# Kernel optimization log

Measured on AMD Instinct MI355X. Metric: run time of the kernel, lower is better.

Reference implementation:

```python
import jax, jax.numpy as jnp
import numpy as np

B, T, J, C = 8, 243, 17, 512
H = 8
HD = C // H  # 64
SCALE = HD ** -0.5


def setup_inputs() -> dict:
    key = jax.random.key(0)
    ks = jax.random.split(key, 6)
    x = jax.random.normal(ks[0], (B, T, J, C), dtype=jnp.float32)
    # external attention map, broadcast-compatible with [B,H,J,T,T]; make it row-normalized like a softmax
    am = jax.random.uniform(ks[1], (B, H, J, T, T), dtype=jnp.float32)
    att_map = am / jnp.sum(am, axis=-1, keepdims=True)
    weight = jax.random.uniform(ks[2], (1,), dtype=jnp.float32)
    w_qkv = jax.random.normal(ks[3], (3 * C, C), dtype=jnp.float32) * 0.02
    w_proj = jax.random.normal(ks[4], (C, C), dtype=jnp.float32) * 0.02
    b_proj = jax.random.normal(ks[5], (C,), dtype=jnp.float32) * 0.02
    return {"x": x, "att_map": att_map, "weight": weight,
            "w_qkv": w_qkv, "w_proj": w_proj, "b_proj": b_proj}


def reference(x, att_map, weight, w_qkv, w_proj, b_proj):
    b, t, j, c = x.shape
    h, hd = H, c // H
    # qkv projection (no bias): [B,T,J,3C] -> [3,B,H,T,J,hd]
    qkv = jnp.einsum('btjc,dc->btjd', x, w_qkv).reshape(b, t, j, 3, h, hd)
    qkv = jnp.transpose(qkv, (3, 0, 4, 1, 2, 5))
    q, k, v = qkv[0], qkv[1], qkv[2]
    # transpose T <-> J: attention runs over the temporal axis per joint
    qt = jnp.swapaxes(q, 2, 3)  # [B,H,J,T,hd]
    kt = jnp.swapaxes(k, 2, 3)
    vt = jnp.swapaxes(v, 2, 3)
    attn = jnp.einsum('bhjtc,bhjsc->bhjts', qt, kt) * SCALE  # [B,H,J,T,T]
    attn = jax.nn.softmax(attn, axis=-1)
    # blend with external attention map (dropout p=0.0 -> identity)
    attn = weight * attn + (1.0 - weight) * att_map
    out = jnp.einsum('bhjts,bhjsc->bhjtc', attn, vt)  # [B,H,J,T,hd]
    out = jnp.transpose(out, (0, 3, 2, 1, 4)).reshape(b, t, j, c)  # [B,T,J,C]
    out = out @ w_proj.T + b_proj
    return out
```

## Files before the change

kernel.cpp:

```cpp
#include <hip/hip_runtime.h>
#include <hip/hip_bf16.h>

#define B_ 8
#define T_ 243
#define J_ 17
#define C_ 512
#define H_ 8
#define HD_ 64
#define M_ (B_*T_*J_)
#define SCALE_ 0.125f
#define QKV_ELEMS (B_*H_*J_*T_*HD_)

typedef __attribute__((ext_vector_type(4))) float f32x4;
typedef __attribute__((ext_vector_type(8))) short bf16x8;

__device__ __forceinline__ ushort f2bf(float f) {
  union { float f; unsigned u; } v; v.f = f;
  unsigned r = v.u + 0x7FFFu + ((v.u >> 16) & 1u);
  return (ushort)(r >> 16);
}
__device__ __forceinline__ float bf2f(ushort u) {
  union { unsigned u; float f; } v; v.u = (unsigned)u << 16; return v.f;
}

__global__ __launch_bounds__(256) void cvt_kernel(const float* __restrict__ in,
                                                  ushort* __restrict__ out, int n8) {
  int i = blockIdx.x * 256 + threadIdx.x;
  if (i >= n8) return;
  const float4* p = (const float4*)in + (size_t)i * 2;
  float4 v0 = p[0], v1 = p[1];
  bf16x8 o;
  o[0] = (short)f2bf(v0.x); o[1] = (short)f2bf(v0.y);
  o[2] = (short)f2bf(v0.z); o[3] = (short)f2bf(v0.w);
  o[4] = (short)f2bf(v1.x); o[5] = (short)f2bf(v1.y);
  o[6] = (short)f2bf(v1.z); o[7] = (short)f2bf(v1.w);
  *(bf16x8*)(out + (size_t)i * 8) = o;
}

template<int EPI>
__global__ __launch_bounds__(256) void gemm_bt(
    const ushort* __restrict__ A, const ushort* __restrict__ Bm,
    ushort* __restrict__ qkvout, float* __restrict__ fout,
    const float* __restrict__ bias)
{
  __shared__ ushort As[128 * 64];
  __shared__ ushort Bs[128 * 64];
  const int tid = threadIdx.x;
  const int lane = tid & 63;
  const int lo = lane & 15, hi = lane >> 4;
  const int wave = tid >> 6;
  const int wr = wave >> 1, wc = wave & 1;
  const int mt = blockIdx.x, nt = blockIdx.y;

  f32x4 acc[4][4] = {};

  for (int ks = 0; ks < 8; ++ks) {
    const int k0 = ks * 64;
    bf16x8 ra[4], rb[4];
    #pragma unroll
    for (int i = 0; i < 4; ++i) {
      int c = tid + i * 256;
      int row = c >> 3, col8 = c & 7;
      int arow = mt * 128 + row; if (arow > M_ - 1) arow = M_ - 1;
      ra[i] = *(const bf16x8*)(A + (size_t)arow * 512 + k0 + col8 * 8);
      int brow = nt * 128 + row;
      rb[i] = *(const bf16x8*)(Bm + (size_t)brow * 512 + k0 + col8 * 8);
    }
    __syncthreads();
    #pragma unroll
    for (int i = 0; i < 4; ++i) {
      int c = tid + i * 256;
      int row = c >> 3, col8 = c & 7;
      int sc = col8 ^ (row & 7);
      *(bf16x8*)(As + row * 64 + sc * 8) = ra[i];
      *(bf16x8*)(Bs + row * 64 + sc * 8) = rb[i];
    }
    __syncthreads();
    #pragma unroll
    for (int kk = 0; kk < 2; ++kk) {
      bf16x8 af[4], bf[4];
      #pragma unroll
      for (int mf = 0; mf < 4; ++mf) {
        int row = wr * 64 + mf * 16 + lo;
        int sc = (kk * 4 + hi) ^ (row & 7);
        af[mf] = *(const bf16x8*)(As + row * 64 + sc * 8);
      }
      #pragma unroll
      for (int nf = 0; nf < 4; ++nf) {
        int row = wc * 64 + nf * 16 + lo;
        int sc = (kk * 4 + hi) ^ (row & 7);
        bf[nf] = *(const bf16x8*)(Bs + row * 64 + sc * 8);
      }
      #pragma unroll
      for (int mf = 0; mf < 4; ++mf)
        #pragma unroll
        for (int nf = 0; nf < 4; ++nf)
          acc[mf][nf] = __builtin_amdgcn_mfma_f32_16x16x32_bf16(af[mf], bf[nf], acc[mf][nf], 0, 0, 0);
    }
  }

  if (EPI == 0) {
    const int which = nt >> 2;
    const int h = (nt * 2 + wc) & 7;
    const float scale = (which == 0) ? SCALE_ : 1.0f;
    ushort* basep = qkvout + (size_t)which * QKV_ELEMS;
    #pragma unroll
    for (int mf = 0; mf < 4; ++mf) {
      #pragma unroll
      for (int i = 0; i < 4; ++i) {
        int r = mt * 128 + wr * 64 + mf * 16 + hi * 4 + i;
        if (r >= M_) continue;
        int b = r / (T_ * J_);
        int rem = r - b * (T_ * J_);
        int t = rem / J_;
        int j = rem - t * J_;
        size_t rowoff = (((size_t)(b * H_ + h) * J_ + j) * T_ + t) * HD_;
        #pragma unroll
        for (int nf = 0; nf < 4; ++nf) {
          int hd = nf * 16 + lo;
          basep[rowoff + hd] = f2bf(acc[mf][nf][i] * scale);
        }
      }
    }
  } else {
    #pragma unroll
    for (int mf = 0; mf < 4; ++mf) {
      #pragma unroll
      for (int i = 0; i < 4; ++i) {
        int r = mt * 128 + wr * 64 + mf * 16 + hi * 4 + i;
        if (r >= M_) continue;
        #pragma unroll
        for (int nf = 0; nf < 4; ++nf) {
          int n = nt * 128 + wc * 64 + nf * 16 + lo;
          fout[(size_t)r * C_ + n] = acc[mf][nf][i] + bias[n];
        }
      }
    }
  }
}

__global__ __launch_bounds__(256, 3) void flash_kernel(
    const ushort* __restrict__ q, const ushort* __restrict__ k,
    const ushort* __restrict__ v, const float* __restrict__ wptr,
    ushort* __restrict__ O2)
{
  __shared__ ushort Vt[64 * 256];
  __shared__ ushort Ps[64 * 128];
  __shared__ float red0[2][64];
  __shared__ float red1[2][64];

  const int tid = threadIdx.x;
  const int lane = tid & 63;
  const int lo = lane & 15, hi = lane >> 4;
  const int wave = tid >> 6;
  const int wr = wave >> 1, wc = wave & 1;
  const int bid = blockIdx.x;
  const int workid = (bid & 7) * 544 + (bid >> 3);
  const int bhj = workid >> 2, rt = workid & 3;
  const float w = wptr[0];
  const size_t kvbase = (size_t)bhj * (T_ * HD_);
  const int r0 = rt * 64;

  #pragma unroll
  for (int it = 0; it < 8; ++it) {
    int c = tid + it * 256;
    int s = c >> 3, hd0 = (c & 7) * 8;
    bf16x8 val = {};
    if (s < T_) val = *(const bf16x8*)(v + kvbase + (size_t)s * HD_ + hd0);
    #pragma unroll
    for (int e = 0; e < 8; ++e) {
      int row = hd0 + e;
      int chunk = (s >> 3) ^ (row & 7);
      Vt[row * 256 + chunk * 8 + (s & 7)] = (ushort)val[e];
    }
  }
  __syncthreads();

  bf16x8 aq[2][2];
  #pragma unroll
  for (int mf = 0; mf < 2; ++mf) {
    int t = r0 + wr * 32 + mf * 16 + lo; if (t > T_ - 1) t = T_ - 1;
    #pragma unroll
    for (int kk = 0; kk < 2; ++kk)
      aq[mf][kk] = *(const bf16x8*)(q + kvbase + (size_t)t * HD_ + kk * 32 + hi * 8);
  }

  f32x4 acc[2][8] = {};
  #pragma unroll
  for (int nf = 0; nf < 8; ++nf) {
    int s = wc * 128 + nf * 16 + lo; if (s > T_ - 1) s = T_ - 1;
    #pragma unroll
    for (int kk = 0; kk < 2; ++kk) {
      bf16x8 bk = *(const bf16x8*)(k + kvbase + (size_t)s * HD_ + kk * 32 + hi * 8);
      #pragma unroll
      for (int mf = 0; mf < 2; ++mf)
        acc[mf][nf] = __builtin_amdgcn_mfma_f32_16x16x32_bf16(aq[mf][kk], bk, acc[mf][nf], 0, 0, 0);
    }
  }

  float rmax[2][4];
  #pragma unroll
  for (int mf = 0; mf < 2; ++mf)
    #pragma unroll
    for (int i = 0; i < 4; ++i) {
      float m = -1e30f;
      #pragma unroll
      for (int nf = 0; nf < 8; ++nf) {
        int s = wc * 128 + nf * 16 + lo;
        if (s < T_) m = fmaxf(m, acc[mf][nf][i]);
      }
      rmax[mf][i] = m;
    }
  #pragma unroll
  for (int d = 1; d < 16; d <<= 1)
    #pragma unroll
    for (int mf = 0; mf < 2; ++mf)
      #pragma unroll
      for (int i = 0; i < 4; ++i)
        rmax[mf][i] = fmaxf(rmax[mf][i], __shfl_xor(rmax[mf][i], d, 64));
  if (lo == 0) {
    #pragma unroll
    for (int mf = 0; mf < 2; ++mf)
      #pragma unroll
      for (int i = 0; i < 4; ++i)
        red0[wc][wr * 32 + mf * 16 + hi * 4 + i] = rmax[mf][i];
  }
  __syncthreads();

  float rsum[2][4];
  #pragma unroll
  for (int mf = 0; mf < 2; ++mf)
    #pragma unroll
    for (int i = 0; i < 4; ++i) {
      float Mx = fmaxf(rmax[mf][i], red0[wc ^ 1][wr * 32 + mf * 16 + hi * 4 + i]);
      float ssum = 0.f;
      #pragma unroll
      for (int nf = 0; nf < 8; ++nf) {
        int s = wc * 128 + nf * 16 + lo;
        float e = 0.f;
        if (s < T_) e = __expf(acc[mf][nf][i] - Mx);
        acc[mf][nf][i] = e;
        ssum += e;
      }
      rsum[mf][i] = ssum;
    }
  #pragma unroll
  for (int d = 1; d < 16; d <<= 1)
    #pragma unroll
    for (int mf = 0; mf < 2; ++mf)
      #pragma unroll
      for (int i = 0; i < 4; ++i)
        rsum[mf][i] += __shfl_xor(rsum[mf][i], d, 64);
  if (lo == 0) {
    #pragma unroll
    for (int mf = 0; mf < 2; ++mf)
      #pragma unroll
      for (int i = 0; i < 4; ++i)
        red1[wc][wr * 32 + mf * 16 + hi * 4 + i] = rsum[mf][i];
  }
  __syncthreads();

  float pinv[2][4];
  #pragma unroll
  for (int mf = 0; mf < 2; ++mf)
    #pragma unroll
    for (int i = 0; i < 4; ++i) {
      float L = rsum[mf][i] + red1[wc ^ 1][wr * 32 + mf * 16 + hi * 4 + i];
      pinv[mf][i] = w / L;
    }

  f32x4 oacc[2][2] = {};
  #pragma unroll
  for (int h2 = 0; h2 < 2; ++h2) {
    __syncthreads();
    if (wc == h2) {
      #pragma unroll
      for (int mf = 0; mf < 2; ++mf)
        #pragma unroll
        for (int i = 0; i < 4; ++i) {
          int row_local = wr * 32 + mf * 16 + hi * 4 + i;
          float pw = pinv[mf][i];
          #pragma unroll
          for (int nf = 0; nf < 8; ++nf) {
            int s = h2 * 128 + nf * 16 + lo;
            float p = (s < T_) ? acc[mf][nf][i] * pw : 0.f;
            int s_local = nf * 16 + lo;
            int chunk = (s_local >> 3) ^ (row_local & 7);
            Ps[row_local * 128 + chunk * 8 + (s_local & 7)] = f2bf(p);
          }
        }
    }
    __syncthreads();
    #pragma unroll
    for (int kk = 0; kk < 4; ++kk) {
      bf16x8 ap[2], bv[2];
      #pragma unroll
      for (int mf = 0; mf < 2; ++mf) {
        int row = wr * 32 + mf * 16 + lo;
        int chunk = (kk * 4 + hi) ^ (row & 7);
        ap[mf] = *(const bf16x8*)(Ps + row * 128 + chunk * 8);
      }
      #pragma unroll
      for (int nf = 0; nf < 2; ++nf) {
        int row = wc * 32 + nf * 16 + lo;
        int chunk = ((h2 * 4 + kk) * 4 + hi) ^ (row & 7);
        bv[nf] = *(const bf16x8*)(Vt + row * 256 + chunk * 8);
      }
      #pragma unroll
      for (int mf = 0; mf < 2; ++mf)
        #pragma unroll
        for (int nf = 0; nf < 2; ++nf)
          oacc[mf][nf] = __builtin_amdgcn_mfma_f32_16x16x32_bf16(ap[mf], bv[nf], oacc[mf][nf], 0, 0, 0);
    }
  }

  #pragma unroll
  for (int mf = 0; mf < 2; ++mf)
    #pragma unroll
    for (int i = 0; i < 4; ++i) {
      int t = r0 + wr * 32 + mf * 16 + hi * 4 + i;
      if (t >= T_) continue;
      size_t rowoff = ((size_t)bhj * T_ + t) * HD_;
      #pragma unroll
      for (int nf = 0; nf < 2; ++nf) {
        int hd = wc * 32 + nf * 16 + lo;
        O2[rowoff + hd] = f2bf(oacc[mf][nf][i]);
      }
    }
}

__global__ __launch_bounds__(256, 4) void amv_kernel(
    const float* __restrict__ am, const ushort* __restrict__ v,
    const ushort* __restrict__ o2, const float* __restrict__ wptr,
    ushort* __restrict__ outO)
{
  __shared__ ushort Vt[64 * 256];

  const int tid = threadIdx.x;
  const int lane = tid & 63;
  const int lo = lane & 15, hi = lane >> 4;
  const int wave = tid >> 6;
  const int wr = wave >> 1, wc = wave & 1;
  const int bid = blockIdx.x;
  const int workid = (bid & 7) * 544 + (bid >> 3);
  const int bhj = workid >> 2, rt = workid & 3;
  const int bh = bhj / J_, j = bhj - bh * J_;
  const int b = bh >> 3, h = bh & 7;
  const float wb = 1.0f - wptr[0];
  const size_t kvbase = (size_t)bhj * (T_ * HD_);
  const int r0 = rt * 64;

  #pragma unroll
  for (int it = 0; it < 8; ++it) {
    int c = tid + it * 256;
    int s = c >> 3, hd0 = (c & 7) * 8;
    bf16x8 val = {};
    if (s < T_) val = *(const bf16x8*)(v + kvbase + (size_t)s * HD_ + hd0);
    #pragma unroll
    for (int e = 0; e < 8; ++e) {
      int row = hd0 + e;
      int chunk = (s >> 3) ^ (row & 7);
      Vt[row * 256 + chunk * 8 + (s & 7)] = (ushort)val[e];
    }
  }
  __syncthreads();

  const float* amrow[2];
  #pragma unroll
  for (int mf = 0; mf < 2; ++mf) {
    int t = r0 + wr * 32 + mf * 16 + lo; if (t > T_ - 1) t = T_ - 1;
    amrow[mf] = am + (size_t)bhj * (T_ * T_) + (size_t)t * T_;
  }

  f32x4 acc[2][2] = {};
  #pragma unroll
  for (int kk = 0; kk < 8; ++kk) {
    const int s8 = kk * 32 + hi * 8;
    bf16x8 aa[2];
    #pragma unroll
    for (int mf = 0; mf < 2; ++mf) {
      bf16x8 r;
      if (s8 + 7 <= T_ - 1) {
        #pragma unroll
        for (int e = 0; e < 8; ++e) r[e] = (short)f2bf(amrow[mf][s8 + e]);
      } else {
        #pragma unroll
        for (int e = 0; e < 8; ++e) {
          int s = s8 + e;
          r[e] = (s <= T_ - 1) ? (short)f2bf(amrow[mf][s]) : (short)0;
        }
      }
      aa[mf] = r;
    }
    bf16x8 bv[2];
    #pragma unroll
    for (int nf = 0; nf < 2; ++nf) {
      int row = wc * 32 + nf * 16 + lo;
      int chunk = (kk * 4 + hi) ^ (row & 7);
      bv[nf] = *(const bf16x8*)(Vt + row * 256 + chunk * 8);
    }
    #pragma unroll
    for (int mf = 0; mf < 2; ++mf)
      #pragma unroll
      for (int nf = 0; nf < 2; ++nf)
        acc[mf][nf] = __builtin_amdgcn_mfma_f32_16x16x32_bf16(aa[mf], bv[nf], acc[mf][nf], 0, 0, 0);
  }

  #pragma unroll
  for (int mf = 0; mf < 2; ++mf)
    #pragma unroll
    for (int i = 0; i < 4; ++i) {
      int t = r0 + wr * 32 + mf * 16 + hi * 4 + i;
      if (t >= T_) continue;
      size_t o2row = ((size_t)bhj * T_ + t) * HD_;
      size_t orow = ((size_t)(b * T_ + t) * J_ + j) * C_ + h * HD_;
      #pragma unroll
      for (int nf = 0; nf < 2; ++nf) {
        int hd = wc * 32 + nf * 16 + lo;
        outO[orow + hd] = f2bf(wb * acc[mf][nf][i] + bf2f(o2[o2row + hd]));
      }
    }
}

extern "C" void kernel_launch(void* const* d_in, const int* in_sizes, int n_in,
                              void* d_out, int out_size, void* d_ws, size_t ws_size,
                              hipStream_t stream) {
  const float* x      = (const float*)d_in[0];
  const float* am     = (const float*)d_in[1];
  const float* weight = (const float*)d_in[2];
  const float* w_qkv  = (const float*)d_in[3];
  const float* w_proj = (const float*)d_in[4];
  const float* b_proj = (const float*)d_in[5];
  float* outp = (float*)d_out;

  char* ws = (char*)d_ws;
  ushort* wqkv_bf  = (ushort*)(ws);
  ushort* wproj_bf = (ushort*)(ws + 1572864);
  ushort* xbf      = (ushort*)(ws + 2097152);
  ushort* qws      = (ushort*)(ws + 35938304);
  ushort* kws = qws + QKV_ELEMS;
  ushort* vws = kws + QKV_ELEMS;
  if (ws_size < 137461760ull) return;

  cvt_kernel<<<8262, 256, 0, stream>>>(x, xbf, 2115072);
  cvt_kernel<<<384, 256, 0, stream>>>(w_qkv, wqkv_bf, 98304);
  cvt_kernel<<<128, 256, 0, stream>>>(w_proj, wproj_bf, 32768);

  gemm_bt<0><<<dim3(259, 12), 256, 0, stream>>>(xbf, wqkv_bf, qws, nullptr, nullptr);

  flash_kernel<<<4352, 256, 0, stream>>>(qws, kws, vws, weight, xbf);

  amv_kernel<<<4352, 256, 0, stream>>>(am, vws, xbf, weight, qws);

  gemm_bt<1><<<dim3(259, 4), 256, 0, stream>>>(qws, wproj_bf, nullptr, outp, b_proj);
}
```

Before: 369.4 us.

## Use direct global-to-LDS loads, exp2 softmax, hardware bf16 convert, and priority hints

The GEMM staging now uses global_load_lds to write tiles straight into shared memory with a pre-swizzled source address, instead of loading into registers and storing them. Softmax folds log2(e) into the Q scale and calls exp2f in place of __expf. The am-matrix conversion uses the packed v_cvt_pk_bf16_f32 instruction in place of manual rounding. The V transpose swizzle gains an extra XOR term to cut LDS bank conflicts, and s_setprio raises wave priority around the MFMA loops. The direct LDS load drops register staging but leaves no double buffering, so load latency is still exposed.

```diff
diff --git a/kernel.cpp b/kernel.cpp
--- a/kernel.cpp
+++ b/kernel.cpp
@@ -9,6 +9,7 @@
 #define HD_ 64
 #define M_ (B_*T_*J_)
 #define SCALE_ 0.125f
+#define SCALE_L2E_ 0.18033688011112042f
 #define QKV_ELEMS (B_*H_*J_*T_*HD_)
 
 typedef __attribute__((ext_vector_type(4))) float f32x4;
@@ -21,6 +22,29 @@
 }
 __device__ __forceinline__ float bf2f(ushort u) {
   union { unsigned u; float f; } v; v.u = (unsigned)u << 16; return v.f;
+}
+__device__ __forceinline__ int vchunk(int g, int row) {
+  return g ^ (row & 7) ^ ((row >> 3) & 7);
+}
+__device__ __forceinline__ void gll16(const void* g, void* l) {
+  __builtin_amdgcn_global_load_lds(
+      (__attribute__((address_space(1))) void*)g,
+      (__attribute__((address_space(3))) void*)l, 16, 0, 0);
+}
+__device__ __forceinline__ bf16x8 load_am_frag(const float* __restrict__ amrow, int s8) {
+  float fv[8];
+  if (s8 + 7 <= T_ - 1) {
+    #pragma unroll
+    for (int e = 0; e < 8; ++e) fv[e] = amrow[s8 + e];
+  } else {
+    #pragma unroll
+    for (int e = 0; e < 8; ++e) { int s = s8 + e; fv[e] = (s <= T_ - 1) ? amrow[s] : 0.f; }
+  }
+  union { bf16x8 v; unsigned u[4]; } r;
+  #pragma unroll
+  for (int p = 0; p < 4; ++p)
+    asm("v_cvt_pk_bf16_f32 %0, %1, %2" : "=v"(r.u[p]) : "v"(fv[2 * p]), "v"(fv[2 * p + 1]));
+  return r.v;
 }
 
 __global__ __launch_bounds__(256) void cvt_kernel(const float* __restrict__ in,
@@ -43,8 +67,8 @@
     ushort* __restrict__ qkvout, float* __restrict__ fout,
     const float* __restrict__ bias)
 {
-  __shared__ ushort As[128 * 64];
-  __shared__ ushort Bs[128 * 64];
+  __shared__ alignas(16) ushort As[128 * 64];
+  __shared__ alignas(16) ushort Bs[128 * 64];
   const int tid = threadIdx.x;
   const int lane = tid & 63;
   const int lo = lane & 15, hi = lane >> 4;
@@ -56,24 +80,22 @@
 
   for (int ks = 0; ks < 8; ++ks) {
     const int k0 = ks * 64;
-    bf16x8 ra[4], rb[4];
+    __syncthreads();
     #pragma unroll
     for (int i = 0; i < 4; ++i) {
       int c = tid + i * 256;
-      int row = c >> 3, col8 = c & 7;
+      int row = c >> 3;
+      int col8g = (c & 7) ^ (row & 7);
       int arow = mt * 128 + row; if (arow > M_ - 1) arow = M_ - 1;
-      ra[i] = *(const bf16x8*)(A + (size_t)arow * 512 + k0 + col8 * 8);
+      gll16(A + (size_t)arow * 512 + k0 + col8g * 8, As + c * 8);
+    }
+    #pragma unroll
+    for (int i = 0; i < 4; ++i) {
+      int c = tid + i * 256;
+      int row = c >> 3;
+      int col8g = (c & 7) ^ (row & 7);
       int brow = nt * 128 + row;
-      rb[i] = *(const bf16x8*)(Bm + (size_t)brow * 512 + k0 + col8 * 8);
-    }
-    __syncthreads();
-    #pragma unroll
-    for (int i = 0; i < 4; ++i) {
-      int c = tid + i * 256;
-      int row = c >> 3, col8 = c & 7;
-      int sc = col8 ^ (row & 7);
-      *(bf16x8*)(As + row * 64 + sc * 8) = ra[i];
-      *(bf16x8*)(Bs + row * 64 + sc * 8) = rb[i];
+      gll16(Bm + (size_t)brow * 512 + k0 + col8g * 8, Bs + c * 8);
     }
     __syncthreads();
     #pragma unroll
@@ -102,7 +124,7 @@
   if (EPI == 0) {
     const int which = nt >> 2;
     const int h = (nt * 2 + wc) & 7;
-    const float scale = (which == 0) ? SCALE_ : 1.0f;
+    const float scale = (which == 0) ? SCALE_L2E_ : 1.0f;
     ushort* basep = qkvout + (size_t)which * QKV_ELEMS;
     #pragma unroll
     for (int mf = 0; mf < 4; ++mf) {
@@ -170,7 +192,7 @@
     #pragma unroll
     for (int e = 0; e < 8; ++e) {
       int row = hd0 + e;
-      int chunk = (s >> 3) ^ (row & 7);
+      int chunk = vchunk(s >> 3, row);
       Vt[row * 256 + chunk * 8 + (s & 7)] = (ushort)val[e];
     }
   }
@@ -186,6 +208,7 @@
   }
 
   f32x4 acc[2][8] = {};
+  __builtin_amdgcn_s_setprio(1);
   #pragma unroll
   for (int nf = 0; nf < 8; ++nf) {
     int s = wc * 128 + nf * 16 + lo; if (s > T_ - 1) s = T_ - 1;
@@ -197,6 +220,7 @@
         acc[mf][nf] = __builtin_amdgcn_mfma_f32_16x16x32_bf16(aq[mf][kk], bk, acc[mf][nf], 0, 0, 0);
     }
   }
+  __builtin_amdgcn_s_setprio(0);
 
   float rmax[2][4];
   #pragma unroll
@@ -238,7 +262,7 @@
       for (int nf = 0; nf < 8; ++nf) {
         int s = wc * 128 + nf * 16 + lo;
         float e = 0.f;
-        if (s < T_) e = __expf(acc[mf][nf][i] - Mx);
+        if (s < T_) e = exp2f(acc[mf][nf][i] - Mx);
         acc[mf][nf][i] = e;
         ssum += e;
       }
@@ -291,6 +315,7 @@
         }
     }
     __syncthreads();
+    __builtin_amdgcn_s_setprio(1);
     #pragma unroll
     for (int kk = 0; kk < 4; ++kk) {
       bf16x8 ap[2], bv[2];
@@ -303,7 +328,7 @@
       #pragma unroll
       for (int nf = 0; nf < 2; ++nf) {
         int row = wc * 32 + nf * 16 + lo;
-        int chunk = ((h2 * 4 + kk) * 4 + hi) ^ (row & 7);
+        int chunk = vchunk((h2 * 4 + kk) * 4 + hi, row);
         bv[nf] = *(const bf16x8*)(Vt + row * 256 + chunk * 8);
       }
       #pragma unroll
@@ -312,6 +337,7 @@
         for (int nf = 0; nf < 2; ++nf)
           oacc[mf][nf] = __builtin_amdgcn_mfma_f32_16x16x32_bf16(ap[mf], bv[nf], oacc[mf][nf], 0, 0, 0);
     }
+    __builtin_amdgcn_s_setprio(0);
   }
 
   #pragma unroll
@@ -359,7 +385,7 @@
     #pragma unroll
     for (int e = 0; e < 8; ++e) {
       int row = hd0 + e;
-      int chunk = (s >> 3) ^ (row & 7);
+      int chunk = vchunk(s >> 3, row);
       Vt[row * 256 + chunk * 8 + (s & 7)] = (ushort)val[e];
     }
   }
@@ -378,26 +404,13 @@
     const int s8 = kk * 32 + hi * 8;
     bf16x8 aa[2];
     #pragma unroll
-    for (int mf = 0; mf < 2; ++mf) {
-      bf16x8 r;
-      if (s8 + 7 <= T_ - 1) {
-        #pragma unroll
-        for (int e = 0; e < 8; ++e) r[e] = (short)f2bf(amrow[mf][s8 + e]);
-      } else {
-        #pragma unroll
-        for (int e = 0; e < 8; ++e) {
-          int s = s8 + e;
-          r[e] = (s <= T_ - 1) ? (short)f2bf(amrow[mf][s]) : (short)0;
-        }
-      }
-      aa[mf] = r;
-    }
+    for (int mf = 0; mf < 2; ++mf)
+      aa[mf] = load_am_frag(amrow[mf], s8);
     bf16x8 bv[2];
     #pragma unroll
     for (int nf = 0; nf < 2; ++nf) {
       int row = wc * 32 + nf * 16 + lo;
-      int chunk = (kk * 4 + hi) ^ (row & 7);
-      bv[nf] = *(const bf16x8*)(Vt + row * 256 + chunk * 8);
+      bv[nf] = *(const bf16x8*)(Vt + row * 256 + vchunk(kk * 4 + hi, row) * 8);
     }
     #pragma unroll
     for (int mf = 0; mf < 2; ++mf)
```

Result: no change. 372.6 us (+0.9%).
